# Performance work log

Hardware: AMD Instinct MI355X
Metric: run time of the kernel (lower is better)

Reference implementation:

```python
import jax, jax.numpy as jnp
import numpy as np
from jax import lax

BETA_CONTENT = 1.0   # content_addressing default beta
BETA_TOPK = 10.0     # top_k_attention default beta
GAMMA = 1.5          # location sharpening
ERASE = 0.5          # erase_strength for write
EPS = 1e-8
NEG = -1.0e9

N_SLOTS, SLOT_D, BATCH, K = 65536, 256, 512, 64


def _l2norm(x):
    # F.normalize: x / max(||x||, 1e-12)
    n = jnp.sqrt(jnp.sum(x * x, axis=-1, keepdims=True))
    return x / jnp.maximum(n, 1e-12)


def setup_inputs() -> dict:
    key = jax.random.key(0)
    k1, k2, k3, k4, k5 = jax.random.split(key, 5)
    return {
        "memory": jax.random.normal(k1, (N_SLOTS, SLOT_D), dtype=jnp.float32) * 0.1,
        "query": jax.random.normal(k2, (BATCH, SLOT_D), dtype=jnp.float32),
        "value": jax.random.normal(k3, (BATCH, SLOT_D), dtype=jnp.float32),
        "prev_weights": jax.random.uniform(k4, (BATCH, N_SLOTS), dtype=jnp.float32),
        "shift_weights": jax.random.uniform(k5, (3,), dtype=jnp.float32),
        "k": K,
    }


def reference(memory, query, value, prev_weights, shift_weights, k):
    B, N = query.shape[0], memory.shape[0]
    # --- content addressing: cosine sim + softmax ---
    qn = _l2norm(query)                      # [B,D]
    mn = _l2norm(memory)                     # [N,D]
    sim = qn @ mn.T                          # [B,N]
    w_content = jax.nn.softmax(BETA_CONTENT * sim, axis=-1)
    read_content = w_content @ memory        # [B,D] read via content weights

    # --- top-k attention: soft threshold mask + softmax ---
    kk = min(int(k), N)
    topk_vals, _ = lax.top_k(sim, kk)        # [B,kk]
    thr = topk_vals[:, -1:]                  # kth largest similarity
    mask = jax.nn.sigmoid(BETA_TOPK * (sim - thr))
    w_topk = jax.nn.softmax(BETA_TOPK * sim + (1.0 - mask) * NEG, axis=-1)
    read_topk = w_topk @ memory              # [B,D]

    # --- location addressing: conv1d shift (padding=1) + gamma sharpen ---
    p = jnp.pad(prev_weights, ((0, 0), (1, 1)))  # [B,N+2]
    shifted = (p[:, :-2] * shift_weights[0]
               + p[:, 1:-1] * shift_weights[1]
               + p[:, 2:] * shift_weights[2])     # [B,N]
    sharp = shifted ** GAMMA
    w_loc = sharp / (jnp.sum(sharp, axis=-1, keepdims=True) + EPS)

    # --- write: softmax(address), multiplicative erase, additive write ---
    w_write = jax.nn.softmax(w_loc, axis=-1)          # write() softmaxes its input
    erase_factor = jnp.prod(1.0 - w_write * ERASE, axis=0)   # [N] sequential erases fused
    new_mem = memory * erase_factor[:, None] + w_write.T @ value  # [N,D]

    return jnp.concatenate([read_content.reshape(-1),
                            read_topk.reshape(-1),
                            new_mem.reshape(-1)])
```

## Files before the change

### kernel.cpp

```cpp
#include <hip/hip_runtime.h>
#include <math.h>

#define BATCH   512
#define NSLOTS  65536
#define DIM     256

#define RB      64
#define NROWG   (BATCH/RB)
#define NCG     64
#define CPG     (NSLOTS/NCG)
#define ST      32
#define NTILES  (CPG/ST)
#define DELTA   0.009f

#define WS_QN   0
#define WS_RN   (WS_QN + BATCH*DIM)
#define WS_WST  (WS_RN + NSLOTS)
#define WS_DEN  (WS_WST + BATCH*4)
#define WS_SST  (WS_DEN + BATCH)
#define WS_VT   (WS_SST + BATCH*NCG*16*4)
#define WS_MN   (WS_VT + (BATCH*DIM)/2)
#define WS_MT   (WS_MN + ((size_t)NSLOTS*DIM)/2)

typedef __attribute__((ext_vector_type(8))) short bf16x8;
typedef __attribute__((ext_vector_type(4))) float f32x4;

__device__ inline unsigned short f2b(float x){
  unsigned u = __float_as_uint(x);
  unsigned r = u + 0x7FFFu + ((u >> 16) & 1u);
  return (unsigned short)(r >> 16);
}
__device__ inline float b2f(unsigned short b){
  return __uint_as_float(((unsigned)b) << 16);
}

__device__ __forceinline__ void gl16(const void* g, void* l){
  __builtin_amdgcn_global_load_lds(
      (__attribute__((address_space(1))) void*)g,
      (__attribute__((address_space(3))) void*)l, 16, 0, 0);
}

#define SBAR_LGKM() do{ asm volatile("s_waitcnt lgkmcnt(0)" ::: "memory"); \
                        __builtin_amdgcn_s_barrier();                      \
                        asm volatile("" ::: "memory"); }while(0)
#define SBAR_ALL()  do{ asm volatile("s_waitcnt vmcnt(0) lgkmcnt(0)" ::: "memory"); \
                        __builtin_amdgcn_s_barrier();                               \
                        asm volatile("" ::: "memory"); }while(0)

__global__ __launch_bounds__(256) void k_qnorm(const float* __restrict__ q, float* __restrict__ qn){
  int b = blockIdx.x, t = threadIdx.x;
  float v = q[b*DIM + t];
  __shared__ float red[256];
  red[t] = v*v;
  __syncthreads();
  for (int s = 128; s > 0; s >>= 1){
    if (t < s) red[t] += red[t+s];
    __syncthreads();
  }
  float n = fmaxf(sqrtf(red[0]), 1e-12f);
  qn[b*DIM + t] = v / n;
}

__global__ __launch_bounds__(256) void k_mnprep(const float* __restrict__ mem,
                                                float* __restrict__ rn,
                                                unsigned short* __restrict__ MN){
  __shared__ float rns[64];
  int t = threadIdx.x;
  int s0 = blockIdx.x * 64;
  int w = t >> 6, ln = t & 63;
  #pragma unroll
  for (int it = 0; it < 16; ++it){
    int r = it*4 + w;
    float4 v = ((const float4*)(mem + (size_t)(s0 + r)*DIM))[ln];
    float s = v.x*v.x + v.y*v.y + v.z*v.z + v.w*v.w;
    #pragma unroll
    for (int off = 32; off > 0; off >>= 1) s += __shfl_xor(s, off, 64);
    if (ln == 0){
      float inv = 1.0f / fmaxf(sqrtf(s), 1e-12f);
      rns[r] = inv; rn[s0 + r] = inv;
    }
  }
  __syncthreads();
  #pragma unroll
  for (int j = 0; j < 8; ++j){
    int id = j*256 + t;
    int r = id >> 5;
    int c = id & 31;
    float inv = rns[r];
    const float4* p = (const float4*)(mem + (size_t)(s0 + r)*DIM + c*8);
    float4 a = p[0], b = p[1];
    bf16x8 o;
    o[0]=(short)f2b(a.x*inv); o[1]=(short)f2b(a.y*inv); o[2]=(short)f2b(a.z*inv); o[3]=(short)f2b(a.w*inv);
    o[4]=(short)f2b(b.x*inv); o[5]=(short)f2b(b.y*inv); o[6]=(short)f2b(b.z*inv); o[7]=(short)f2b(b.w*inv);
    *(bf16x8*)&MN[(size_t)(s0 + r)*DIM + ((c ^ (r & 7))*8)] = o;
  }
}

__global__ __launch_bounds__(256) void k_mtprep(const float* __restrict__ mem, unsigned short* __restrict__ MT){
  __shared__ __align__(16) unsigned short tile[64][68];
  int sb = (blockIdx.x >> 2)*64, dd = (blockIdx.x & 3)*64;
  int t = threadIdx.x;
  int w = t >> 6, ln = t & 63;
  #pragma unroll
  for (int k = 0; k < 4; ++k){
    int sl = w*16 + k*4 + (ln >> 4);
    int doff = (ln & 15)*4;
    float4 f = *(const float4*)&mem[(size_t)(sb + sl)*DIM + dd + doff];
    tile[doff+0][sl] = f2b(f.x);
    tile[doff+1][sl] = f2b(f.y);
    tile[doff+2][sl] = f2b(f.z);
    tile[doff+3][sl] = f2b(f.w);
  }
  __syncthreads();
  #pragma unroll
  for (int k = 0; k < 4; ++k){
    int dl = w*16 + k*4 + (ln >> 4);
    int boff = (ln & 15)*4;
    int B = boff >> 5;
    int p = (boff >> 3) & 3;
    int pp = p ^ ((dl >> 1) & 3);
    int off = B*32 + pp*8 + (boff & 7);
    *(short4*)&MT[(size_t)(dd + dl)*NSLOTS + sb + off] = *(const short4*)&tile[dl][boff];
  }
}

__global__ __launch_bounds__(256) void k_prep(const float* __restrict__ val, unsigned short* __restrict__ VT){
  __shared__ __align__(16) unsigned short tile[64][68];
  int bb = (blockIdx.x >> 2)*64, dd = (blockIdx.x & 3)*64;
  int t = threadIdx.x;
  int w = t >> 6, ln = t & 63;
  #pragma unroll
  for (int k = 0; k < 4; ++k){
    int bl = w*16 + k*4 + (ln >> 4);
    int doff = (ln & 15)*4;
    float4 f = *(const float4*)&val[(size_t)(bb + bl)*DIM + dd + doff];
    tile[doff+0][bl] = f2b(f.x);
    tile[doff+1][bl] = f2b(f.y);
    tile[doff+2][bl] = f2b(f.z);
    tile[doff+3][bl] = f2b(f.w);
  }
  __syncthreads();
  #pragma unroll
  for (int k = 0; k < 4; ++k){
    int dl = w*16 + k*4 + (ln >> 4);
    int boff = (ln & 15)*4;
    *(short4*)&VT[(size_t)(dd + dl)*BATCH + bb + boff] = *(const short4*)&tile[dl][boff];
  }
}

__global__ __launch_bounds__(256) void k_wstats(const float* __restrict__ prev, const float* __restrict__ sw,
                                                float* __restrict__ wst){
  int b = blockIdx.x, t = threadIdx.x;
  float s0 = sw[0], s1 = sw[1], s2 = sw[2];
  const float* p = prev + (size_t)b*NSLOTS;
  const float4* p4 = (const float4*)p;
  __shared__ float rs[256];
  float lsum = 0.f;
  for (int i4 = t; i4 < NSLOTS/4; i4 += 256){
    float4 f = p4[i4];
    float lft = (i4 > 0) ? p[4*i4 - 1] : 0.f;
    float rgt = (i4 < NSLOTS/4 - 1) ? p[4*i4 + 4] : 0.f;
    float sh0 = s0*lft + s1*f.x + s2*f.y;
    float sh1 = s0*f.x + s1*f.y + s2*f.z;
    float sh2 = s0*f.y + s1*f.z + s2*f.w;
    float sh3 = s0*f.z + s1*f.w + s2*rgt;
    lsum += sh0*sqrtf(sh0) + sh1*sqrtf(sh1) + sh2*sqrtf(sh2) + sh3*sqrtf(sh3);
  }
  rs[t] = lsum;
  __syncthreads();
  for (int s = 128; s > 0; s >>= 1){
    if (t < s) rs[t] += rs[t+s];
    __syncthreads();
  }
  float inv_d = 1.0f / (rs[0] + 1e-8f);
  __syncthreads();
  float lz = 0.f;
  for (int i4 = t; i4 < NSLOTS/4; i4 += 256){
    float4 f = p4[i4];
    float lft = (i4 > 0) ? p[4*i4 - 1] : 0.f;
    float rgt = (i4 < NSLOTS/4 - 1) ? p[4*i4 + 4] : 0.f;
    float sh0 = s0*lft + s1*f.x + s2*f.y;
    float sh1 = s0*f.x + s1*f.y + s2*f.z;
    float sh2 = s0*f.y + s1*f.z + s2*f.w;
    float sh3 = s0*f.z + s1*f.w + s2*rgt;
    lz += __expf(sh0*sqrtf(sh0)*inv_d) + __expf(sh1*sqrtf(sh1)*inv_d)
        + __expf(sh2*sqrtf(sh2)*inv_d) + __expf(sh3*sqrtf(sh3)*inv_d);
  }
  rs[t] = lz;
  __syncthreads();
  for (int s = 128; s > 0; s >>= 1){
    if (t < s) rs[t] += rs[t+s];
    __syncthreads();
  }
  if (t == 0){
    float4 o; o.x = inv_d; o.y = 1.0f/rs[0]; o.z = 0.f; o.w = 0.f;
    ((float4*)wst)[b] = o;
  }
}

__global__ __launch_bounds__(256, 2) void k_simfused(
    const float* __restrict__ qn,
    const unsigned short* __restrict__ MN,
    const unsigned short* __restrict__ MT,
    float* __restrict__ outc, float* __restrict__ denom, float* __restrict__ sst)
{
  __shared__ __align__(16) unsigned short Ms[2][32*256];
  __shared__ __align__(16) unsigned short Md[2][256*32];
  __shared__ __align__(16) unsigned short Plds[64*40];

  int cg = blockIdx.x, rg = blockIdx.y;
  int t = threadIdx.x;
  int w = t >> 6;
  int lane = t & 63;
  int l = lane & 15;
  int q = lane >> 4;
  int row0 = rg * RB;

  bf16x8 qa[8];
  {
    int qrow = row0 + 16*w + l;
    #pragma unroll
    for (int kk = 0; kk < 8; ++kk){
      const float4* qp = (const float4*)&qn[(size_t)qrow*DIM + 32*kk + 8*q];
      float4 a0 = qp[0], a1 = qp[1];
      bf16x8 v;
      v[0]=(short)f2b(a0.x); v[1]=(short)f2b(a0.y); v[2]=(short)f2b(a0.z); v[3]=(short)f2b(a0.w);
      v[4]=(short)f2b(a1.x); v[5]=(short)f2b(a1.y); v[6]=(short)f2b(a1.z); v[7]=(short)f2b(a1.w);
      qa[kk] = v;
    }
  }

  const char* msP = (const char*)MN + (size_t)cg*CPG*512 + (size_t)w*4096 + (size_t)lane*16;
  const char* mtP = (const char*)MT + (size_t)(w*64 + (lane>>2))*((size_t)NSLOTS*2)
                                    + (size_t)cg*CPG*2 + (size_t)(lane&3)*16;

  auto STAGE = [&](int tl, int buf){
    size_t mso = (size_t)tl*16384;
    size_t mto = (size_t)tl*64;
    #pragma unroll
    for (int j = 0; j < 4; ++j)
      gl16(msP + mso + (size_t)j*1024, &Ms[buf][w*2048 + j*512]);
    #pragma unroll
    for (int j = 0; j < 4; ++j)
      gl16(mtP + mto + (size_t)j*2097152, &Md[buf][w*2048 + j*512]);
  };

  f32x4 accO[16];
  #pragma unroll
  for (int c = 0; c < 16; ++c) accO[c] = (f32x4){0.f,0.f,0.f,0.f};

  float dsum[4] = {0.f,0.f,0.f,0.f};
  float tv0[4] = {-1e30f,-1e30f,-1e30f,-1e30f}, tv1[4] = {-1e30f,-1e30f,-1e30f,-1e30f};
  int   ti0[4] = {0,0,0,0}, ti1[4] = {0,0,0,0};

  STAGE(0, 0);
  SBAR_ALL();

  int r7 = l & 7;
  int sw2 = (q ^ ((l >> 1) & 3)) * 8;

  for (int tile = 0; tile < NTILES; ++tile){
    int cur = tile & 1;
    if (tile + 1 < NTILES) STAGE(tile + 1, cur ^ 1);
    int i0 = cg*CPG + tile*ST;

    const unsigned short* msb = &Ms[cur][0];
    f32x4 S0 = (f32x4){0.f,0.f,0.f,0.f}, S1 = (f32x4){0.f,0.f,0.f,0.f};
    #pragma unroll
    for (int kk = 0; kk < 8; ++kk){
      int c0 = ((4*kk + q) ^ r7) * 8;
      bf16x8 b0 = *(const bf16x8*)&msb[(l     )*256 + c0];
      bf16x8 b1 = *(const bf16x8*)&msb[(16 + l)*256 + c0];
      S0 = __builtin_amdgcn_mfma_f32_16x16x32_bf16(qa[kk], b0, S0, 0, 0, 0);
      S1 = __builtin_amdgcn_mfma_f32_16x16x32_bf16(qa[kk], b1, S1, 0, 0, 0);
    }

    #pragma unroll
    for (int c = 0; c < 2; ++c){
      int slot = i0 + 16*c + l;
      #pragma unroll
      for (int reg = 0; reg < 4; ++reg){
        float v = (c == 0) ? S0[reg] : S1[reg];
        bool g0 = v > tv0[reg];
        bool g1 = v > tv1[reg];
        float ov0 = tv0[reg]; int oi0 = ti0[reg];
        tv1[reg] = g0 ? ov0 : (g1 ? v : tv1[reg]);
        ti1[reg] = g0 ? oi0 : (g1 ? slot : ti1[reg]);
        tv0[reg] = g0 ? v : tv0[reg];
        ti0[reg] = g0 ? slot : ti0[reg];
        unsigned short wb = f2b(__expf(v));
        dsum[reg] += b2f(wb);
        Plds[(16*w + 4*q + reg)*40 + 16*c + l] = (short)wb;
      }
    }
    SBAR_LGKM();

    bf16x8 pa = *(const bf16x8*)&Plds[(16*w + l)*40 + 8*q];
    const unsigned short* mdb = &Md[cur][0];
    #pragma unroll
    for (int ct = 0; ct < 16; ++ct){
      bf16x8 b = *(const bf16x8*)&mdb[(16*ct + l)*32 + sw2];
      accO[ct] = __builtin_amdgcn_mfma_f32_16x16x32_bf16(pa, b, accO[ct], 0, 0, 0);
    }
    SBAR_ALL();
  }

  #pragma unroll
  for (int reg = 0; reg < 4; ++reg){
    float s = dsum[reg];
    s += __shfl_xor(s, 1, 64); s += __shfl_xor(s, 2, 64);
    s += __shfl_xor(s, 4, 64); s += __shfl_xor(s, 8, 64);
    if (l == 0) atomicAdd(&denom[row0 + 16*w + 4*q + reg], s);
  }
  #pragma unroll
  for (int reg = 0; reg < 4; ++reg){
    int row = row0 + 16*w + 4*q + reg;
    size_t base = (((size_t)row*NCG + cg)*16 + l)*2;
    float2* S2 = (float2*)sst;
    S2[base + 0] = make_float2(tv0[reg], __int_as_float(ti0[reg]));
    S2[base + 1] = make_float2(tv1[reg], __int_as_float(ti1[reg]));
  }
  #pragma unroll
  for (int ct = 0; ct < 16; ++ct){
    #pragma unroll
    for (int reg = 0; reg < 4; ++reg){
      int row = row0 + 16*w + 4*q + reg;
      atomicAdd(&outc[(size_t)row*DIM + 16*ct + l], accO[ct][reg]);
    }
  }
}

__global__ __launch_bounds__(256) void k_finish(const float* __restrict__ sst, const float* __restrict__ denom,
                                                const float* __restrict__ qn, const float* __restrict__ rn,
                                                const float* __restrict__ mem,
                                                float* __restrict__ outc, float* __restrict__ outk){
  int row = blockIdx.x, t = threadIdx.x;
  __shared__ float red[256];
  __shared__ int cnt;
  __shared__ int cidx[128];
  __shared__ float csim[128];
  __shared__ int bestIdx;
  const float2* S = (const float2*)sst + (size_t)row*NCG*16*2;
  float2 e[8];
  float lmax = -1e30f;
  #pragma unroll
  for (int k = 0; k < 8; ++k){ e[k] = S[t*8 + k]; lmax = fmaxf(lmax, e[k].x); }
  red[t] = lmax;
  __syncthreads();
  for (int s = 128; s > 0; s >>= 1){
    if (t < s) red[t] = fmaxf(red[t], red[t+s]);
    __syncthreads();
  }
  float M = red[0];
  if (t == 0) cnt = 0;
  __syncthreads();
  #pragma unroll
  for (int k = 0; k < 8; ++k){
    if (e[k].x >= M - DELTA){
      int p = atomicAdd(&cnt, 1);
      if (p < 128) cidx[p] = __float_as_int(e[k].y);
    }
  }
  __syncthreads();
  int n = min(cnt, 128);
  int wv = t >> 6, ln = t & 63;
  for (int ci = wv; ci < n; ci += 4){
    int slot = cidx[ci];
    float4 a = ((const float4*)&qn[(size_t)row*DIM])[ln];
    float4 b = ((const float4*)&mem[(size_t)slot*DIM])[ln];
    float s = a.x*b.x + a.y*b.y + a.z*b.z + a.w*b.w;
    #pragma unroll
    for (int off = 32; off > 0; off >>= 1) s += __shfl_xor(s, off, 64);
    if (ln == 0) csim[ci] = s * rn[slot];
  }
  __syncthreads();
  if (t == 0){
    float bv = -1e30f; int bi = 0x7fffffff;
    for (int i = 0; i < n; ++i){
      float v = csim[i]; int id = cidx[i];
      if (v > bv || (v == bv && id < bi)){ bv = v; bi = id; }
    }
    bestIdx = bi;
  }
  __syncthreads();
  float inv = 1.0f / denom[row];
  outc[(size_t)row*DIM + t] *= inv;
  outk[(size_t)row*DIM + t] = mem[(size_t)bestIdx*DIM + t];
}

__global__ __launch_bounds__(256, 4) void k_newmem(const float* __restrict__ mem,
                                                const unsigned short* __restrict__ VT,
                                                const float* __restrict__ prev, const float* __restrict__ sw,
                                                const float* __restrict__ wst, float* __restrict__ outm){
  int t = threadIdx.x;
  int i0 = blockIdx.x * 64;
  int w = t >> 6;
  int lane = t & 63;
  int l = lane & 15, q = lane >> 4;
  int slot = i0 + 16*w + l;
  float s0 = sw[0], s1 = sw[1], s2 = sw[2];

  f32x4 accO[16];
  #pragma unroll
  for (int c = 0; c < 16; ++c) accO[c] = (f32x4){0.f,0.f,0.f,0.f};
  float epl = 1.0f;

  const float* pc = prev + (size_t)slot;

  #pragma unroll 1
  for (int c = 0; c < 16; ++c){
    bf16x8 af;
    #pragma unroll
    for (int j = 0; j < 8; ++j){
      int b = c*32 + q*8 + j;
      const float* p = pc + (size_t)b*NSLOTS;
      float a  = (slot > 0) ? p[-1] : 0.f;
      float ce = p[0];
      float d  = (slot < NSLOTS-1) ? p[1] : 0.f;
      float sh = s0*a + s1*ce + s2*d;
      float sharp = sh*sqrtf(sh);
      float2 st = *(const float2*)&wst[b*4];
      float wf = __expf(sharp*st.x)*st.y;
      epl *= (1.0f - 0.5f*wf);
      af[j] = (short)f2b(wf);
    }
    #pragma unroll
    for (int ct = 0; ct < 16; ++ct){
      bf16x8 bfg = *(const bf16x8*)&VT[(size_t)(16*ct + l)*BATCH + c*32 + 8*q];
      accO[ct] = __builtin_amdgcn_mfma_f32_16x16x32_bf16(af, bfg, accO[ct], 0, 0, 0);
    }
  }

  epl *= __shfl_xor(epl, 16, 64);
  epl *= __shfl_xor(epl, 32, 64);

  #pragma unroll
  for (int reg = 0; reg < 4; ++reg){
    int so = i0 + 16*w + 4*q + reg;
    float e = __shfl(epl, 4*q + reg, 64);
    #pragma unroll
    for (int ct = 0; ct < 16; ++ct){
      int d = 16*ct + l;
      outm[(size_t)so*DIM + d] = mem[(size_t)so*DIM + d]*e + accO[ct][reg];
    }
  }
}

extern "C" void kernel_launch(void* const* d_in, const int* in_sizes, int n_in,
                              void* d_out, int out_size, void* d_ws, size_t ws_size,
                              hipStream_t stream){
  const float* mem  = (const float*)d_in[0];
  const float* qry  = (const float*)d_in[1];
  const float* val  = (const float*)d_in[2];
  const float* prev = (const float*)d_in[3];
  const float* sw   = (const float*)d_in[4];
  float* out = (float*)d_out;
  float* ws  = (float*)d_ws;

  float* qn   = ws + WS_QN;
  float* rn   = ws + WS_RN;
  float* wst  = ws + WS_WST;
  float* den  = ws + WS_DEN;
  float* sst  = ws + WS_SST;
  unsigned short* VT = (unsigned short*)(ws + WS_VT);
  unsigned short* MN = (unsigned short*)(ws + WS_MN);
  unsigned short* MT = (unsigned short*)(ws + WS_MT);

  float* out_content = out;
  float* out_topk    = out + BATCH*DIM;
  float* out_newmem  = out + 2*BATCH*DIM;

  hipMemsetAsync(out_content, 0, BATCH*DIM*sizeof(float), stream);
  hipMemsetAsync(den, 0, BATCH*sizeof(float), stream);
  hipLaunchKernelGGL(k_qnorm,   dim3(BATCH),       dim3(DIM), 0, stream, qry, qn);
  hipLaunchKernelGGL(k_mnprep,  dim3(NSLOTS/64),   dim3(256), 0, stream, mem, rn, MN);
  hipLaunchKernelGGL(k_mtprep,  dim3((NSLOTS/64)*4), dim3(256), 0, stream, mem, MT);
  hipLaunchKernelGGL(k_prep,    dim3(32),          dim3(256), 0, stream, val, VT);
  hipLaunchKernelGGL(k_wstats,  dim3(BATCH),       dim3(256), 0, stream, prev, sw, wst);
  hipLaunchKernelGGL(k_simfused,dim3(NCG, NROWG),  dim3(256), 0, stream, qn, MN, MT, out_content, den, sst);
  hipLaunchKernelGGL(k_finish,  dim3(BATCH),       dim3(256), 0, stream, sst, den, qn, rn, mem, out_content, out_topk);
  hipLaunchKernelGGL(k_newmem,  dim3(NSLOTS/64),   dim3(256), 0, stream, mem, VT, prev, sw, wst, out_newmem);
}
```

Baseline: 611.9 us.

## Precompute transposed bf16 write weights in separate kernel before newmem

Adds a kernel that computes the shifted, sharpened, exponentiated write weights from prev_weights in coalesced row order, transposes them through shared memory, and stores them as bf16 slot-major into the reused MN workspace. k_newmem then loads contiguous bf16x8 vectors instead of doing strided per-element reads of prev across batch rows with recomputation. The aim is to get rid of the uncoalesced strided access pattern in k_newmem. The cost is an extra kernel launch and an extra 64MB bf16 write and read. The erase product is now computed from bf16-rounded weights, which slightly lowers precision.

```diff
diff --git a/kernel.cpp b/kernel.cpp
--- a/kernel.cpp
+++ b/kernel.cpp
@@ -198,6 +198,45 @@
   }
 }
 
+__global__ __launch_bounds__(256) void k_wft(const float* __restrict__ prev, const float* __restrict__ sw,
+                                             const float* __restrict__ wst, unsigned short* __restrict__ WFT){
+  __shared__ __align__(16) unsigned short T[64][72];
+  int bs = ((int)blockIdx.x & 7) * 64;
+  int ss = ((int)blockIdx.x >> 3) * 64;
+  int t = threadIdx.x;
+  float s0 = sw[0], s1 = sw[1], s2 = sw[2];
+  int rr = t >> 4;
+  int cc = t & 15;
+  #pragma unroll
+  for (int pass = 0; pass < 4; ++pass){
+    int bl = pass*16 + rr;
+    int b = bs + bl;
+    const float* p = prev + (size_t)b*NSLOTS + ss;
+    float2 st = *(const float2*)&wst[b*4];
+    int s = cc*4;
+    float4 f = *(const float4*)(p + s);
+    int gs = ss + s;
+    float lft = (gs > 0) ? p[s-1] : 0.f;
+    float rgt = (gs + 4 < NSLOTS) ? p[s+4] : 0.f;
+    float sh0 = s0*lft + s1*f.x + s2*f.y;
+    float sh1 = s0*f.x + s1*f.y + s2*f.z;
+    float sh2 = s0*f.y + s1*f.z + s2*f.w;
+    float sh3 = s0*f.z + s1*f.w + s2*rgt;
+    T[s+0][bl] = f2b(__expf(sh0*sqrtf(sh0)*st.x)*st.y);
+    T[s+1][bl] = f2b(__expf(sh1*sqrtf(sh1)*st.x)*st.y);
+    T[s+2][bl] = f2b(__expf(sh2*sqrtf(sh2)*st.x)*st.y);
+    T[s+3][bl] = f2b(__expf(sh3*sqrtf(sh3)*st.x)*st.y);
+  }
+  __syncthreads();
+  int sr = t >> 3;
+  int ch = t & 7;
+  #pragma unroll
+  for (int k = 0; k < 2; ++k){
+    int row = k*32 + sr;
+    *(bf16x8*)&WFT[(size_t)(ss + row)*BATCH + bs + ch*8] = *(const bf16x8*)&T[row][ch*8];
+  }
+}
+
 __global__ __launch_bounds__(256, 2) void k_simfused(
     const float* __restrict__ qn,
     const unsigned short* __restrict__ MN,
@@ -390,40 +429,28 @@
 
 __global__ __launch_bounds__(256, 4) void k_newmem(const float* __restrict__ mem,
                                                 const unsigned short* __restrict__ VT,
-                                                const float* __restrict__ prev, const float* __restrict__ sw,
-                                                const float* __restrict__ wst, float* __restrict__ outm){
+                                                const unsigned short* __restrict__ WFT,
+                                                float* __restrict__ outm){
   int t = threadIdx.x;
   int i0 = blockIdx.x * 64;
   int w = t >> 6;
   int lane = t & 63;
   int l = lane & 15, q = lane >> 4;
   int slot = i0 + 16*w + l;
-  float s0 = sw[0], s1 = sw[1], s2 = sw[2];
 
   f32x4 accO[16];
   #pragma unroll
   for (int c = 0; c < 16; ++c) accO[c] = (f32x4){0.f,0.f,0.f,0.f};
   float epl = 1.0f;
 
-  const float* pc = prev + (size_t)slot;
-
-  #pragma unroll 1
+  const unsigned short* wrow = WFT + (size_t)slot*BATCH;
+
+  #pragma unroll 2
   for (int c = 0; c < 16; ++c){
-    bf16x8 af;
-    #pragma unroll
-    for (int j = 0; j < 8; ++j){
-      int b = c*32 + q*8 + j;
-      const float* p = pc + (size_t)b*NSLOTS;
-      float a  = (slot > 0) ? p[-1] : 0.f;
-      float ce = p[0];
-      float d  = (slot < NSLOTS-1) ? p[1] : 0.f;
-      float sh = s0*a + s1*ce + s2*d;
-      float sharp = sh*sqrtf(sh);
-      float2 st = *(const float2*)&wst[b*4];
-      float wf = __expf(sharp*st.x)*st.y;
-      epl *= (1.0f - 0.5f*wf);
-      af[j] = (short)f2b(wf);
-    }
+    bf16x8 af = *(const bf16x8*)&wrow[c*32 + 8*q];
+    #pragma unroll
+    for (int j = 0; j < 8; ++j)
+      epl *= (1.0f - 0.5f*b2f((unsigned short)af[j]));
     #pragma unroll
     for (int ct = 0; ct < 16; ++ct){
       bf16x8 bfg = *(const bf16x8*)&VT[(size_t)(16*ct + l)*BATCH + c*32 + 8*q];
@@ -465,6 +492,7 @@
   unsigned short* VT = (unsigned short*)(ws + WS_VT);
   unsigned short* MN = (unsigned short*)(ws + WS_MN);
   unsigned short* MT = (unsigned short*)(ws + WS_MT);
+  unsigned short* WFT = MN;
 
   float* out_content = out;
   float* out_topk    = out + BATCH*DIM;
@@ -478,6 +506,7 @@
   hipLaunchKernelGGL(k_prep,    dim3(32),          dim3(256), 0, stream, val, VT);
   hipLaunchKernelGGL(k_wstats,  dim3(BATCH),       dim3(256), 0, stream, prev, sw, wst);
   hipLaunchKernelGGL(k_simfused,dim3(NCG, NROWG),  dim3(256), 0, stream, qn, MN, MT, out_content, den, sst);
+  hipLaunchKernelGGL(k_wft,     dim3((NSLOTS/64)*(BATCH/64)), dim3(256), 0, stream, prev, sw, wst, WFT);
   hipLaunchKernelGGL(k_finish,  dim3(BATCH),       dim3(256), 0, stream, sst, den, qn, rn, mem, out_content, out_topk);
-  hipLaunchKernelGGL(k_newmem,  dim3(NSLOTS/64),   dim3(256), 0, stream, mem, VT, prev, sw, wst, out_newmem);
-}
+  hipLaunchKernelGGL(k_newmem,  dim3(NSLOTS/64),   dim3(256), 0, stream, mem, VT, WFT, out_newmem);
+}
```

After: 621.5 us. About the same (+1.6%).
